# Kernel optimization log

Hardware: AMD Instinct MI355X
Metric: run time of the kernel (lower is better)

The kernel has to match this reference:

```python
import jax, jax.numpy as jnp
import numpy as np

N_RAYS = 262144
N_SAMPLES = 128
NEAR, FAR = 0.0, 1.0
FAR_DELTA = 1e10  # sentinel delta for last sample


def setup_inputs() -> dict:
    key = jax.random.key(0)
    k1, k2, k3 = jax.random.split(key, 3)
    rgb = jax.random.uniform(k1, (N_RAYS, N_SAMPLES, 3), dtype=jnp.float32)
    density = jax.random.uniform(k2, (N_RAYS, N_SAMPLES, 1), dtype=jnp.float32)
    # distances must be increasing along sample axis, in [near, far]
    t = jax.random.uniform(k3, (N_RAYS, N_SAMPLES), dtype=jnp.float32)
    distances = NEAR + (FAR - NEAR) * jnp.sort(t, axis=-1)
    return {"rgb": rgb, "density": density, "distances": distances}


def reference(rgb, density, distances):
    # delta_i = t_{i+1} - t_i, last delta = 1e10
    delta = jnp.concatenate(
        [distances[..., 1:] - distances[..., :-1],
         jnp.full_like(distances[..., :1], FAR_DELTA)], axis=-1)
    alpha = 1.0 - jnp.exp(-density[..., 0] * delta)          # [N, S]
    # exclusive cumprod of (1 - alpha) -> transmittance
    transmittance = jnp.cumprod(
        jnp.concatenate([jnp.ones_like(alpha[..., :1]), 1.0 - alpha[..., :-1]], axis=-1),
        axis=-1)
    weights = alpha * transmittance                           # [N, S]
    rendered_rgb = jnp.sum(weights[..., None] * rgb, axis=-2)  # [N, 3]
    return rendered_rgb
```

## Files before the change

### kernel.cpp

```cpp
#include <hip/hip_runtime.h>


#define FAR_DELTA 1e10f

__global__ __launch_bounds__(64) void volrender_kernel(
    const float* __restrict__ rgb,
    const float* __restrict__ density,
    const float* __restrict__ dist,
    float* __restrict__ out,
    int n_rays)
{
    const int t  = threadIdx.x;
    const int r0 = blockIdx.x << 6;

    __shared__ float SIG[64 * 12];
    __shared__ float DST[64 * 12];
    __shared__ float RGBT[64 * 28];

    const int    ray  = min(r0 + t, n_rays - 1);
    const size_t rowD = (size_t)ray * 128;

    float T    = 1.0f;
    float accR = 0.0f, accG = 0.0f, accB = 0.0f;

    for (int tile = 0; tile < 16; ++tile) {
        const int s0 = tile << 3;

        #pragma unroll
        for (int k = 0; k < 2; ++k) {
            const int    j   = t + (k << 6);
            const int    row = j >> 1;
            const int    col = (j & 1) << 2;
            const int    gr  = min(r0 + row, n_rays - 1);
            const size_t g   = (size_t)gr * 128 + s0 + col;
            const float4 sv  = *(const float4*)(density + g);
            const float4 dv  = *(const float4*)(dist + g);
            *(float4*)(&SIG[row * 12 + col]) = sv;
            *(float4*)(&DST[row * 12 + col]) = dv;
        }
        #pragma unroll
        for (int k = 0; k < 6; ++k) {
            const int    j   = t + (k << 6);
            const int    row = j / 6;
            const int    col = (j - row * 6) << 2;
            const int    gr  = min(r0 + row, n_rays - 1);
            const size_t g   = (size_t)gr * 384 + (size_t)s0 * 3 + col;
            *(float4*)(&RGBT[row * 28 + col]) = *(const float4*)(rgb + g);
        }
        const float d_carry = dist[rowD + min(s0 + 8, 127)];

        __syncthreads();

        const float4 sg0 = *(const float4*)(&SIG[t * 12]);
        const float4 sg1 = *(const float4*)(&SIG[t * 12 + 4]);
        const float4 dv0 = *(const float4*)(&DST[t * 12]);
        const float4 dv1 = *(const float4*)(&DST[t * 12 + 4]);

        float cf[24];
        #pragma unroll
        for (int k = 0; k < 6; ++k) {
            const float4 v = *(const float4*)(&RGBT[t * 28 + (k << 2)]);
            cf[(k << 2) + 0] = v.x;  cf[(k << 2) + 1] = v.y;
            cf[(k << 2) + 2] = v.z;  cf[(k << 2) + 3] = v.w;
        }

        const float dl[9] = {dv0.x, dv0.y, dv0.z, dv0.w,
                             dv1.x, dv1.y, dv1.z, dv1.w, d_carry};
        const float sl[8] = {sg0.x, sg0.y, sg0.z, sg0.w,
                             sg1.x, sg1.y, sg1.z, sg1.w};

        #pragma unroll
        for (int j = 0; j < 8; ++j) {
            const float delta = (s0 + j == 127) ? FAR_DELTA : (dl[j + 1] - dl[j]);
            const float e = __expf(-sl[j] * delta);
            const float w = T - T * e;
            T *= e;
            accR += w * cf[3 * j + 0];
            accG += w * cf[3 * j + 1];
            accB += w * cf[3 * j + 2];
        }

        __syncthreads();
    }

    if (r0 + t < n_rays) {
        float* o = out + (size_t)(r0 + t) * 3;
        o[0] = accR;
        o[1] = accG;
        o[2] = accB;
    }
}

extern "C" void kernel_launch(void* const* d_in, const int* in_sizes, int n_in,
                              void* d_out, int out_size, void* d_ws, size_t ws_size,
                              hipStream_t stream) {
    const float* rgb     = (const float*)d_in[0];
    const float* density = (const float*)d_in[1];
    const float* dist    = (const float*)d_in[2];
    float* out = (float*)d_out;

    const int n_rays = in_sizes[2] / 128;

    const int block = 64;
    const int grid  = (n_rays + 63) / 64;

    volrender_kernel<<<grid, block, 0, stream>>>(rgb, density, dist, out, n_rays);
}
```

Baseline: 735.7 us.

## Double-buffer global loads in registers and carry last sample across tiles

Global loads for the density, distance and RGB tiles are now issued one tile ahead into two register buffers, then committed to shared memory while the previous tile is computed. This overlaps memory latency with the exponential and accumulation math. The last sample of each tile is carried into the next tile, which removes the extra per-ray global load for the boundary distance and the per-sample FAR_DELTA check. The __syncthreads barriers are dropped, relying on the 64-thread block being a single wavefront. The absence of any LDS fence risks the compiler reordering shared-memory accesses, and the added register buffers may cost occupancy.

```diff
diff --git a/kernel.cpp b/kernel.cpp
--- a/kernel.cpp
+++ b/kernel.cpp
@@ -17,70 +17,96 @@
     __shared__ float DST[64 * 12];
     __shared__ float RGBT[64 * 28];
 
-    const int    ray  = min(r0 + t, n_rays - 1);
-    const size_t rowD = (size_t)ray * 128;
+    const int r_a = t >> 1;            const int c_a = (t & 1) << 2;
+    const int r_b = 32 + (t >> 1);     const int c_b = c_a;
+    const int gra = min(r0 + r_a, n_rays - 1);
+    const int grb = min(r0 + r_b, n_rays - 1);
+    const float* sigpa = density + (size_t)gra * 128 + c_a;
+    const float* sigpb = density + (size_t)grb * 128 + c_b;
+    const float* dstpa = dist    + (size_t)gra * 128 + c_a;
+    const float* dstpb = dist    + (size_t)grb * 128 + c_b;
 
-    float T    = 1.0f;
-    float accR = 0.0f, accG = 0.0f, accB = 0.0f;
+    const float* rgbp[6];
+    int rrow[6], rcol[6];
+    #pragma unroll
+    for (int k = 0; k < 6; ++k) {
+        const int j   = t + (k << 6);
+        const int row = j / 6;
+        const int col = (j - row * 6) << 2;
+        rrow[k] = row; rcol[k] = col;
+        const int gr  = min(r0 + row, n_rays - 1);
+        rgbp[k] = rgb + (size_t)gr * 384 + col;
+    }
 
-    for (int tile = 0; tile < 16; ++tile) {
-        const int s0 = tile << 3;
+    float T = 1.0f, accR = 0.0f, accG = 0.0f, accB = 0.0f;
+    float sig_p = 0.0f, d_p = 0.0f, cr_p = 0.0f, cg_p = 0.0f, cb_p = 0.0f;
 
+    auto issue = [&](float4* R, int s0) {
+        R[0] = *(const float4*)(sigpa + s0);
+        R[1] = *(const float4*)(sigpb + s0);
+        R[2] = *(const float4*)(dstpa + s0);
+        R[3] = *(const float4*)(dstpb + s0);
         #pragma unroll
-        for (int k = 0; k < 2; ++k) {
-            const int    j   = t + (k << 6);
-            const int    row = j >> 1;
-            const int    col = (j & 1) << 2;
-            const int    gr  = min(r0 + row, n_rays - 1);
-            const size_t g   = (size_t)gr * 128 + s0 + col;
-            const float4 sv  = *(const float4*)(density + g);
-            const float4 dv  = *(const float4*)(dist + g);
-            *(float4*)(&SIG[row * 12 + col]) = sv;
-            *(float4*)(&DST[row * 12 + col]) = dv;
-        }
+        for (int k = 0; k < 6; ++k)
+            R[4 + k] = *(const float4*)(rgbp[k] + s0 * 3);
+    };
+    auto commit = [&](const float4* R) {
+        *(float4*)&SIG[r_a * 12 + c_a] = R[0];
+        *(float4*)&SIG[r_b * 12 + c_b] = R[1];
+        *(float4*)&DST[r_a * 12 + c_a] = R[2];
+        *(float4*)&DST[r_b * 12 + c_b] = R[3];
         #pragma unroll
-        for (int k = 0; k < 6; ++k) {
-            const int    j   = t + (k << 6);
-            const int    row = j / 6;
-            const int    col = (j - row * 6) << 2;
-            const int    gr  = min(r0 + row, n_rays - 1);
-            const size_t g   = (size_t)gr * 384 + (size_t)s0 * 3 + col;
-            *(float4*)(&RGBT[row * 28 + col]) = *(const float4*)(rgb + g);
-        }
-        const float d_carry = dist[rowD + min(s0 + 8, 127)];
-
-        __syncthreads();
-
-        const float4 sg0 = *(const float4*)(&SIG[t * 12]);
-        const float4 sg1 = *(const float4*)(&SIG[t * 12 + 4]);
-        const float4 dv0 = *(const float4*)(&DST[t * 12]);
-        const float4 dv1 = *(const float4*)(&DST[t * 12 + 4]);
-
+        for (int k = 0; k < 6; ++k)
+            *(float4*)&RGBT[rrow[k] * 28 + rcol[k]] = R[4 + k];
+    };
+    auto compute = [&](int s0) {
+        const float4 sg0 = *(const float4*)&SIG[t * 12];
+        const float4 sg1 = *(const float4*)&SIG[t * 12 + 4];
+        const float4 dv0 = *(const float4*)&DST[t * 12];
+        const float4 dv1 = *(const float4*)&DST[t * 12 + 4];
         float cf[24];
         #pragma unroll
         for (int k = 0; k < 6; ++k) {
-            const float4 v = *(const float4*)(&RGBT[t * 28 + (k << 2)]);
-            cf[(k << 2) + 0] = v.x;  cf[(k << 2) + 1] = v.y;
-            cf[(k << 2) + 2] = v.z;  cf[(k << 2) + 3] = v.w;
+            const float4 v = *(const float4*)&RGBT[t * 28 + (k << 2)];
+            cf[4*k] = v.x; cf[4*k+1] = v.y; cf[4*k+2] = v.z; cf[4*k+3] = v.w;
         }
+        const float dl[8] = {dv0.x,dv0.y,dv0.z,dv0.w, dv1.x,dv1.y,dv1.z,dv1.w};
+        const float sl[8] = {sg0.x,sg0.y,sg0.z,sg0.w, sg1.x,sg1.y,sg1.z,sg1.w};
 
-        const float dl[9] = {dv0.x, dv0.y, dv0.z, dv0.w,
-                             dv1.x, dv1.y, dv1.z, dv1.w, d_carry};
-        const float sl[8] = {sg0.x, sg0.y, sg0.z, sg0.w,
-                             sg1.x, sg1.y, sg1.z, sg1.w};
-
-        #pragma unroll
-        for (int j = 0; j < 8; ++j) {
-            const float delta = (s0 + j == 127) ? FAR_DELTA : (dl[j + 1] - dl[j]);
-            const float e = __expf(-sl[j] * delta);
+        {
+            const float e = __expf(-sig_p * (dl[0] - d_p));
             const float w = T - T * e;
             T *= e;
-            accR += w * cf[3 * j + 0];
-            accG += w * cf[3 * j + 1];
-            accB += w * cf[3 * j + 2];
+            accR += w * cr_p; accG += w * cg_p; accB += w * cb_p;
         }
+        #pragma unroll
+        for (int j = 0; j < 7; ++j) {
+            const float e = __expf(-sl[j] * (dl[j + 1] - dl[j]));
+            const float w = T - T * e;
+            T *= e;
+            accR += w * cf[3*j + 0]; accG += w * cf[3*j + 1]; accB += w * cf[3*j + 2];
+        }
+        sig_p = sl[7]; d_p = dl[7];
+        cr_p = cf[21]; cg_p = cf[22]; cb_p = cf[23];
+        (void)s0;
+    };
 
-        __syncthreads();
+    float4 A[10], B[10];
+    issue(A, 0);
+    #pragma unroll
+    for (int kk = 0; kk < 8; ++kk) {
+        commit(A);
+        issue(B, (2 * kk + 1) * 8);
+        compute(2 * kk * 8);
+        commit(B);
+        if (kk < 7) issue(A, (2 * kk + 2) * 8);
+        compute((2 * kk + 1) * 8);
+    }
+
+    {
+        const float e = __expf(-sig_p * FAR_DELTA);
+        const float w = T - T * e;
+        accR += w * cr_p; accG += w * cg_p; accB += w * cb_p;
     }
 
     if (r0 + t < n_rays) {
```

New measurement: 813.4 us. +10.6%, slower.
